# Performance work log

Measured on AMD Instinct MI355X. Metric: run time of the kernel, lower is better.

## Reference

```python
import jax, jax.numpy as jnp
import numpy as np
from jax import lax

# dims: B batch, V views, D feature dim, C classes, P prompts
B, V, D, C, P = 512, 10, 1024, 100, 4
ADAPTER_RATIO = 0.6
EPS = 0.01          # sinkhorn entropic regularizer (compute_logits default)
MAX_ITER = 1000     # compute_logits default
THRESH = 1e-2       # PLOT Sinkhorn early-stop threshold on |r - r_prev|.mean()
BN_EPS = 1e-5


def setup_inputs() -> dict:
    key = jax.random.key(0)
    ks = jax.random.split(key, 8)
    # Correlated features so cosine similarity ~0.9 (realistic CLIP-like sims);
    # keeps exp(-wdist/0.01) well inside fp32 range for the Sinkhorn solver.
    base = jax.random.normal(ks[0], (D,), jnp.float32)
    feat = base[None, :] + 0.3 * jax.random.normal(ks[1], (B * V, D), jnp.float32)
    text_feat = base[None, None, :] + 0.3 * jax.random.normal(ks[2], (C, P, D), jnp.float32)
    w = lambda k, shp: 0.02 * jax.random.normal(k, shp, jnp.float32)
    return {
        "feat": feat,                       # (B*V, D) CLIP visual features
        "text_feat": text_feat,             # (C, P, D) encoded text features
        "fusion_ratio": jnp.full((V,), 0.5, jnp.float32),
        "bn1_gamma": jnp.ones((D,), jnp.float32),
        "bn1_beta": jnp.zeros((D,), jnp.float32),
        "W_glob": w(ks[3], (D, D * V)),     # Linear(D*V -> D), torch layout (out, in)
        "b_glob": jnp.zeros((D,), jnp.float32),
        "bn2_gamma": jnp.ones((D,), jnp.float32),
        "bn2_beta": jnp.zeros((D,), jnp.float32),
        "W_v1": w(ks[4], (D, D)),           # Linear(D -> D)
        "b_v1": jnp.zeros((D,), jnp.float32),
        "W_v2": w(ks[5], (D * V, D)),       # Linear(D -> D*V)
        "b_v2": jnp.zeros((D * V,), jnp.float32),
        "logit_scale": jnp.array(np.log(1.0 / 0.07), jnp.float32),
    }


def _bn_train(x, gamma, beta):
    # BatchNorm1d in training mode: biased batch statistics over axis 0
    m = x.mean(axis=0)
    v = x.var(axis=0)
    return (x - m) * lax.rsqrt(v + BN_EPS) * gamma + beta


def _adapter(feat, fusion_ratio, bn1_g, bn1_b, Wg, bg, bn2_g, bn2_b, Wv1, bv1, Wv2, bv2):
    img = feat.reshape(-1, V, D)
    res = feat.reshape(-1, V * D)
    x = img * fusion_ratio.reshape(1, -1, 1)          # per-view fusion weights
    x = _bn_train(x.reshape(-1, D), bn1_g, bn1_b)     # BatchNormPoint over D
    x = x.reshape(-1, V * D)                          # Flatten
    g = jax.nn.relu(_bn_train(x @ Wg.T + bg, bn2_g, bn2_b))   # global_f (dropout=0)
    view = jax.nn.relu(jax.nn.relu(g @ Wv1.T + bv1) @ Wv2.T + bv2)  # view_f
    return view * ADAPTER_RATIO + res * (1.0 - ADAPTER_RATIO)


def _sinkhorn(K, p, q):
    # PLOT-style Sinkhorn: r = p / (K c); c = q / (K^T r); early stop on mean |dr|
    r0 = jnp.ones_like(p)
    c0 = jnp.ones_like(q)

    def cond(st):
        i, r, c, err = st
        return jnp.logical_and(i < MAX_ITER, err > THRESH)

    def body(st):
        i, r, c, _ = st
        r_prev = r
        r = p / jnp.einsum('nvp,np->nv', K, c)
        c = q / jnp.einsum('nvp,nv->np', K, r)
        err = jnp.mean(jnp.abs(r - r_prev))
        return i + 1, r, c, err

    _, r, c, _ = lax.while_loop(cond, body, (jnp.int32(0), r0, c0, jnp.float32(jnp.inf)))
    return r[:, :, None] * K * c[:, None, :]   # T = diag(r) K diag(c)


def reference(feat, text_feat, fusion_ratio, bn1_gamma, bn1_beta, W_glob, b_glob,
              bn2_gamma, bn2_beta, W_v1, b_v1, W_v2, b_v2, logit_scale):
    img_feat = _adapter(feat, fusion_ratio, bn1_gamma, bn1_beta, W_glob, b_glob,
                        bn2_gamma, bn2_beta, W_v1, b_v1, W_v2, b_v2)
    img_feat = img_feat.reshape(-1, V, D)
    img_feat = img_feat / jnp.linalg.norm(img_feat, axis=-1, keepdims=True)
    txt = text_feat / jnp.linalg.norm(text_feat, axis=-1, keepdims=True)

    # compute_logits: sim (B, C, V, P) -> (B*C, V, P)
    sim = jnp.einsum('bvd,cpd->bcvp', img_feat, txt).reshape(B * C, V, P)
    wdist = 1.0 - sim
    p = jnp.full((B * C, V), 1.0 / V, sim.dtype)
    q = jnp.full((B * C, P), 1.0 / P, sim.dtype)
    K = jnp.exp(-wdist / EPS)
    T = _sinkhorn(lax.stop_gradient(K), p, q)   # solver runs under no_grad
    d_OT = jnp.sum(T * wdist, axis=(1, 2)).reshape(B, C)
    logits = jnp.exp(logit_scale) * (1.0 - d_OT)
    return logits
```

## Files before the change

### kernel.cpp

```cpp
#include <hip/hip_runtime.h>
#include <cstdint>


typedef unsigned short u16;
typedef __attribute__((ext_vector_type(8))) short bf8v;
typedef __attribute__((ext_vector_type(4))) float f4v;

__device__ __forceinline__ float4 ld4(const float* p){ return *reinterpret_cast<const float4*>(p); }
__device__ __forceinline__ void st4(float* p, float4 v){ *reinterpret_cast<float4*>(p) = v; }
__device__ __forceinline__ u16 f2bf(float x){
  uint32_t u = __float_as_uint(x);
  return (u16)((u + 0x7FFFu + ((u>>16)&1u)) >> 16);
}
__device__ __forceinline__ void glds16(const u16* g, u16* l){
  __builtin_amdgcn_global_load_lds(
      (const __attribute__((address_space(1))) unsigned int*)g,
      (__attribute__((address_space(3))) unsigned int*)l, 16, 0, 0);
}

__global__ __launch_bounds__(256,3)
void gemm_bf16_nt(const u16* __restrict__ A, const u16* __restrict__ B,
                  float* __restrict__ C, int lda, int ldb, int ldc,
                  int kLen, long strideCz)
{
  __shared__ u16 As0[4096], Bs0[4096], As1[4096], Bs1[4096];
  const int tid = threadIdx.x, lane = tid & 63, w = tid >> 6;
  const long bm = (long)blockIdx.y*128, bn = (long)blockIdx.x*128;
  const long kz = (long)blockIdx.z*kLen;
  C += (long)blockIdx.z*strideCz;

  const int srow  = lane>>2;
  const int sslot = (lane&3) ^ ((lane>>3)&3);
  const u16* Ag = A + (bm + w*32 + srow)*(long)lda + kz + sslot*8;
  const u16* Bg = B + (bn + w*32 + srow)*(long)ldb + kz + sslot*8;
  const long a16 = 16L*lda, b16 = 16L*ldb;
  const int woff = w*1024;

  const int fr = lane & 15;
  const int rslot = ((lane>>4) ^ ((lane>>1)&3))*16;
  const int wr = (w>>1)*64, wc = (w&1)*64;

  const f4v zero = {0.f,0.f,0.f,0.f};
  f4v acc[4][4];
  #pragma unroll
  for (int i=0;i<4;i++)
    #pragma unroll
    for (int j=0;j<4;j++) acc[i][j]=zero;

  auto STAGE = [&](u16* Al, u16* Bl, int kt){
    glds16(Ag + kt,       Al + woff);
    glds16(Ag + kt + a16, Al + woff + 512);
    glds16(Bg + kt,       Bl + woff);
    glds16(Bg + kt + b16, Bl + woff + 512);
  };
  auto COMPUTE = [&](const u16* Asb, const u16* Bsb){
    bf8v af[4], bf[4];
    #pragma unroll
    for (int mi=0; mi<4; ++mi)
      af[mi] = *(const bf8v*)((const char*)Asb + (wr+mi*16+fr)*64 + rslot);
    #pragma unroll
    for (int nj=0; nj<4; ++nj)
      bf[nj] = *(const bf8v*)((const char*)Bsb + (wc+nj*16+fr)*64 + rslot);
    #pragma unroll
    for (int mi=0; mi<4; ++mi)
      #pragma unroll
      for (int nj=0; nj<4; ++nj)
        acc[mi][nj] = __builtin_amdgcn_mfma_f32_16x16x32_bf16(af[mi], bf[nj], acc[mi][nj], 0,0,0);
  };

  STAGE(As0, Bs0, 0);
  __syncthreads();
  int kt = 32;
  for (; kt < kLen - 32; kt += 64){
    STAGE(As1, Bs1, kt);
    COMPUTE(As0, Bs0);
    __syncthreads();
    STAGE(As0, Bs0, kt + 32);
    COMPUTE(As1, Bs1);
    __syncthreads();
  }
  STAGE(As1, Bs1, kt);
  COMPUTE(As0, Bs0);
  __syncthreads();
  COMPUTE(As1, Bs1);

  const int orow = (lane>>4)*4;
  #pragma unroll
  for (int mi=0;mi<4;++mi){
    #pragma unroll
    for (int q=0;q<4;++q){
      const long row = bm + wr + mi*16 + orow + q;
      float* Crow = C + row*(long)ldc + bn + wc + fr;
      #pragma unroll
      for (int nj=0;nj<4;++nj) Crow[nj*16] = acc[mi][nj][q];
    }
  }
}

__global__ __launch_bounds__(256)
void cvt_bf16(const float* __restrict__ in, u16* __restrict__ out, long n8)
{
  for (long i = (long)blockIdx.x*256 + threadIdx.x; i < n8; i += (long)gridDim.x*256){
    const float4 a = ld4(&in[i*8]), b = ld4(&in[i*8+4]);
    uint4 o;
    o.x = f2bf(a.x) | ((uint32_t)f2bf(a.y)<<16);
    o.y = f2bf(a.z) | ((uint32_t)f2bf(a.w)<<16);
    o.z = f2bf(b.x) | ((uint32_t)f2bf(b.y)<<16);
    o.w = f2bf(b.z) | ((uint32_t)f2bf(b.w)<<16);
    *reinterpret_cast<uint4*>(&out[i*8]) = o;
  }
}

__global__ __launch_bounds__(256)
void reduce_f32(const float* __restrict__ P, int S, int MN,
                const float* __restrict__ bias, float* __restrict__ out)
{
  const long i = ((long)blockIdx.x*256 + threadIdx.x)*4;
  float4 s = ld4(&P[i]);
  for (int z=1; z<S; ++z){
    const float4 v = ld4(&P[(long)z*MN + i]);
    s.x+=v.x; s.y+=v.y; s.z+=v.z; s.w+=v.w;
  }
  const float4 b = ld4(&bias[(int)(i & 1023)]);
  s.x+=b.x; s.y+=b.y; s.z+=b.z; s.w+=b.w;
  st4(&out[i], s);
}

__global__ __launch_bounds__(256)
void reduce_bf16(const float* __restrict__ P, int S, int MN,
                 const float* __restrict__ bias, u16* __restrict__ out)
{
  const long i = ((long)blockIdx.x*256 + threadIdx.x)*4;
  float4 s = ld4(&P[i]);
  for (int z=1; z<S; ++z){
    const float4 v = ld4(&P[(long)z*MN + i]);
    s.x+=v.x; s.y+=v.y; s.z+=v.z; s.w+=v.w;
  }
  const float4 b = ld4(&bias[(int)(i & 1023)]);
  s.x = fmaxf(s.x+b.x,0.f); s.y = fmaxf(s.y+b.y,0.f);
  s.z = fmaxf(s.z+b.z,0.f); s.w = fmaxf(s.w+b.w,0.f);
  uint2 o; o.x = f2bf(s.x) | ((uint32_t)f2bf(s.y)<<16);
  o.y = f2bf(s.z) | ((uint32_t)f2bf(s.w)<<16);
  *reinterpret_cast<uint2*>(&out[i]) = o;
}

__global__ __launch_bounds__(256)
void colstats_p1(const float* __restrict__ X, int rpb, const float* __restrict__ fr,
                 float* __restrict__ part)
{
  const int c = threadIdx.x*4;
  const long r0 = (long)blockIdx.x*rpb;
  float4 s = make_float4(0,0,0,0), q = make_float4(0,0,0,0);
  for (int rr=0; rr<rpb; ++rr){
    const long r = r0+rr;
    float4 x = ld4(&X[r*1024 + c]);
    if (fr){ const float f = fr[(int)(r%10)]; x.x*=f; x.y*=f; x.z*=f; x.w*=f; }
    s.x+=x.x; s.y+=x.y; s.z+=x.z; s.w+=x.w;
    q.x+=x.x*x.x; q.y+=x.y*x.y; q.z+=x.z*x.z; q.w+=x.w*x.w;
  }
  float* p = part + (long)blockIdx.x*2048;
  st4(&p[c], s);
  st4(&p[1024+c], q);
}

__global__ __launch_bounds__(256)
void colstats_reduce(const float* __restrict__ in, float* __restrict__ out,
                     int nslab, int chunk)
{
  const int idx = blockIdx.x*256 + threadIdx.x;
  const int s0 = blockIdx.y*chunk;
  const int s1 = min(nslab, s0+chunk);
  float a0=0.f, a1=0.f, a2=0.f, a3=0.f;
  int s = s0;
  for (; s+4 <= s1; s += 4){
    a0 += in[(long)s*2048+idx];
    a1 += in[(long)(s+1)*2048+idx];
    a2 += in[(long)(s+2)*2048+idx];
    a3 += in[(long)(s+3)*2048+idx];
  }
  for (; s < s1; ++s) a0 += in[(long)s*2048+idx];
  out[(long)blockIdx.y*2048 + idx] = (a0+a1)+(a2+a3);
}

__global__ __launch_bounds__(256)
void bn_apply_bf16(const float* __restrict__ X, const float* __restrict__ fr,
                   const float* __restrict__ stats, float invN,
                   const float* __restrict__ gamma,
                   const float* __restrict__ beta, int relu, u16* __restrict__ out)
{
  const long i = ((long)blockIdx.x*256 + threadIdx.x)*4;
  const int d = (int)(i & 1023);
  const float4 s  = ld4(&stats[d]);
  const float4 qq = ld4(&stats[1024+d]);
  const float4 gm = ld4(&gamma[d]);
  const float4 bt = ld4(&beta[d]);
  float4 sc, sh;
  { const float m=s.x*invN, v=qq.x*invN-m*m; sc.x=gm.x*rsqrtf(v+1e-5f); sh.x=bt.x-m*sc.x; }
  { const float m=s.y*invN, v=qq.y*invN-m*m; sc.y=gm.y*rsqrtf(v+1e-5f); sh.y=bt.y-m*sc.y; }
  { const float m=s.z*invN, v=qq.z*invN-m*m; sc.z=gm.z*rsqrtf(v+1e-5f); sh.z=bt.z-m*sc.z; }
  { const float m=s.w*invN, v=qq.w*invN-m*m; sc.w=gm.w*rsqrtf(v+1e-5f); sh.w=bt.w-m*sc.w; }
  float4 x = ld4(&X[i]);
  if (fr){ const float f = fr[(int)((i>>10)%10)]; x.x*=f; x.y*=f; x.z*=f; x.w*=f; }
  x.x = x.x*sc.x + sh.x; x.y = x.y*sc.y + sh.y;
  x.z = x.z*sc.z + sh.z; x.w = x.w*sc.w + sh.w;
  if (relu){ x.x=fmaxf(x.x,0.f); x.y=fmaxf(x.y,0.f); x.z=fmaxf(x.z,0.f); x.w=fmaxf(x.w,0.f); }
  uint2 o; o.x = f2bf(x.x) | ((uint32_t)f2bf(x.y)<<16);
  o.y = f2bf(x.z) | ((uint32_t)f2bf(x.w)<<16);
  *reinterpret_cast<uint2*>(&out[i]) = o;
}

__device__ __forceinline__ float blockSum256(float v, float* sh4){
  #pragma unroll
  for (int m=32; m; m>>=1) v += __shfl_xor(v, m, 64);
  const int w = threadIdx.x >> 6;
  if ((threadIdx.x & 63) == 0) sh4[w] = v;
  __syncthreads();
  return sh4[0]+sh4[1]+sh4[2]+sh4[3];
}

__global__ __launch_bounds__(256)
void rownorm_bf16(const float* __restrict__ X, u16* __restrict__ out)
{
  __shared__ float sh4[4];
  const int row = blockIdx.x;
  const int d = threadIdx.x*4;
  if (row >= 400){ *reinterpret_cast<uint2*>(&out[(long)row*1024 + d]) = make_uint2(0,0); return; }
  const long base = (long)row*1024 + d;
  const float4 x = ld4(&X[base]);
  const float ss = x.x*x.x + x.y*x.y + x.z*x.z + x.w*x.w;
  const float rn = rsqrtf(blockSum256(ss, sh4));
  uint2 o; o.x = f2bf(x.x*rn) | ((uint32_t)f2bf(x.y*rn)<<16);
  o.y = f2bf(x.z*rn) | ((uint32_t)f2bf(x.w*rn)<<16);
  *reinterpret_cast<uint2*>(&out[base]) = o;
}

__global__ __launch_bounds__(256)
void mix_norm_bf16(const float* __restrict__ P, const float* __restrict__ feat,
                   const float* __restrict__ bv2, u16* __restrict__ outp)
{
  __shared__ float sh4[4];
  const int m = blockIdx.x;
  const int v = m % 10;
  const long base = (long)m*1024;
  const int d = threadIdx.x*4;
  const float4 y  = ld4(&P[base+d]);
  const float4 bb = ld4(&bv2[v*1024 + d]);
  const float4 f  = ld4(&feat[base+d]);
  float4 img;
  img.x = 0.6f*fmaxf(y.x+bb.x,0.f) + 0.4f*f.x;
  img.y = 0.6f*fmaxf(y.y+bb.y,0.f) + 0.4f*f.y;
  img.z = 0.6f*fmaxf(y.z+bb.z,0.f) + 0.4f*f.z;
  img.w = 0.6f*fmaxf(y.w+bb.w,0.f) + 0.4f*f.w;
  const float ss = img.x*img.x + img.y*img.y + img.z*img.z + img.w*img.w;
  const float rn = rsqrtf(blockSum256(ss, sh4));
  uint2 o; o.x = f2bf(img.x*rn) | ((uint32_t)f2bf(img.y*rn)<<16);
  o.y = f2bf(img.z*rn) | ((uint32_t)f2bf(img.w*rn)<<16);
  *reinterpret_cast<uint2*>(&outp[base+d]) = o;
}

__global__ __launch_bounds__(256)
void sinkhorn_scan(const float* __restrict__ sim, float* __restrict__ errb)
{
  const int n = blockIdx.x*256 + threadIdx.x;
  const int b = n / 100, c = n % 100;
  const int bin = (n >> 6) & 63;
  float Km[10][4];
  #pragma unroll
  for (int v=0; v<10; ++v){
    const float4 s4 = ld4(&sim[(long)(b*10+v)*512 + c*4]);
    Km[v][0]=expf((s4.x-1.f)*100.f); Km[v][1]=expf((s4.y-1.f)*100.f);
    Km[v][2]=expf((s4.z-1.f)*100.f); Km[v][3]=expf((s4.w-1.f)*100.f);
  }
  float r[10], cc[4];
  #pragma unroll
  for (int v=0;v<10;++v) r[v]=1.f;
  #pragma unroll
  for (int p=0;p<4;++p) cc[p]=1.f;
  bool done=false;
  for (int j=0; j<1000; ++j){
    float lerr = 0.f;
    if (!done){
      #pragma unroll
      for (int v=0;v<10;++v){
        const float s = Km[v][0]*cc[0]+Km[v][1]*cc[1]+Km[v][2]*cc[2]+Km[v][3]*cc[3];
        const float rn = __fdividef(0.1f, s);
        lerr += fabsf(rn - r[v]); r[v]=rn;
      }
      #pragma unroll
      for (int p=0;p<4;++p){
        float s = 0.f;
        #pragma unroll
        for (int v=0;v<10;++v) s += Km[v][p]*r[v];
        cc[p] = __fdividef(0.25f, s);
      }
      if (lerr == 0.f) done = true;
    }
    float w = lerr;
    #pragma unroll
    for (int m=32; m; m>>=1) w += __shfl_xor(w, m, 64);
    if ((threadIdx.x & 63) == 0 && w > 0.f) atomicAdd(&errb[j*64 + bin], w);
    if (w <= 0.4f) break;
  }
}

__global__ __launch_bounds__(256)
void find_kstar(const float* __restrict__ errb, int* __restrict__ kstar)
{
  __shared__ int best[256];
  const int t = threadIdx.x;
  int loc = 1000000;
  for (int j=t; j<1000; j+=256){
    float s = 0.f;
    #pragma unroll
    for (int u=0; u<64; ++u) s += errb[j*64+u];
    if (s * (1.f/512000.f) <= 0.01f) loc = min(loc, j);
  }
  best[t]=loc; __syncthreads();
  for (int s=128; s; s>>=1){ if (t<s) best[t]=min(best[t],best[t+s]); __syncthreads(); }
  if (t==0) kstar[0] = (best[0]==1000000) ? 1000 : (best[0]+1);
}

__global__ __launch_bounds__(256)
void sinkhorn_final(const float* __restrict__ sim, const int* __restrict__ kstar,
                    const float* __restrict__ lsp, float* __restrict__ out)
{
  const int n = blockIdx.x*256 + threadIdx.x;
  const int b = n / 100, c = n % 100;
  float S[10][4], Km[10][4];
  #pragma unroll
  for (int v=0; v<10; ++v){
    const float4 s4 = ld4(&sim[(long)(b*10+v)*512 + c*4]);
    S[v][0]=s4.x; S[v][1]=s4.y; S[v][2]=s4.z; S[v][3]=s4.w;
    #pragma unroll
    for (int p=0;p<4;++p) Km[v][p] = expf((S[v][p]-1.f)*100.f);
  }
  const int kmax = kstar[0];
  float r[10], cc[4];
  #pragma unroll
  for (int v=0;v<10;++v) r[v]=1.f;
  #pragma unroll
  for (int p=0;p<4;++p) cc[p]=1.f;
  for (int j=0; j<kmax; ++j){
    float lerr = 0.f;
    #pragma unroll
    for (int v=0;v<10;++v){
      const float s = Km[v][0]*cc[0]+Km[v][1]*cc[1]+Km[v][2]*cc[2]+Km[v][3]*cc[3];
      const float rn = __fdividef(0.1f, s);
      lerr += fabsf(rn - r[v]); r[v]=rn;
    }
    #pragma unroll
    for (int p=0;p<4;++p){
      float s = 0.f;
      #pragma unroll
      for (int v=0;v<10;++v) s += Km[v][p]*r[v];
      cc[p] = __fdividef(0.25f, s);
    }
    if (lerr == 0.f) break;
  }
  float dOT = 0.f;
  #pragma unroll
  for (int v=0;v<10;++v)
    #pragma unroll
    for (int p=0;p<4;++p)
      dOT += r[v]*Km[v][p]*cc[p]*(1.f - S[v][p]);
  out[n] = expf(lsp[0]) * (1.f - dOT);
}

extern "C" void kernel_launch(void* const* d_in, const int* in_sizes, int n_in,
                              void* d_out, int out_size, void* d_ws, size_t ws_size,
                              hipStream_t stream)
{
  const float* feat  = (const float*)d_in[0];
  const float* textf = (const float*)d_in[1];
  const float* fr    = (const float*)d_in[2];
  const float* bn1g  = (const float*)d_in[3];
  const float* bn1b  = (const float*)d_in[4];
  const float* Wg    = (const float*)d_in[5];
  const float* bg    = (const float*)d_in[6];
  const float* bn2g  = (const float*)d_in[7];
  const float* bn2b  = (const float*)d_in[8];
  const float* Wv1   = (const float*)d_in[9];
  const float* bv1   = (const float*)d_in[10];
  const float* Wv2   = (const float*)d_in[11];
  const float* bv2   = (const float*)d_in[12];
  const float* ls    = (const float*)d_in[13];
  float* out = (float*)d_out;
  char* base = (char*)d_ws;

  u16*   Wb  = (u16*)(base + 0);
  u16*   Xb  = (u16*)(base + 20971520);
  float* P   = (float*)(base + 31457280);
  float* P2  = P + 1310720;
  u16*   W1b = (u16*)(base + 65011712);
  float* y1  = (float*)(base + 67108864);
  u16*   Gb  = (u16*)(base + 69206016);
  u16*   Hb  = (u16*)(base + 70254592);
  u16*   Tb  = (u16*)(base + 71303168);
  float* ex  = (float*)(base + 72351744);
  float* bn1st=ex, *bn2st=ex+2048;
  float* errb = ex+8192;
  int*   kstar= (int*)(ex+8192+64000);

  hipMemsetAsync(errb, 0, 64000*sizeof(float), stream);

  cvt_bf16<<<2048,256,0,stream>>>(Wg, Wb, 1310720);

  colstats_p1<<<640,256,0,stream>>>(feat, 8, fr, P);
  colstats_reduce<<<dim3(8,20),256,0,stream>>>(P, P2, 640, 32);
  colstats_reduce<<<dim3(8,1),256,0,stream>>>(P2, bn1st, 20, 20);
  bn_apply_bf16<<<5120,256,0,stream>>>(feat, fr, bn1st, 1.f/5120.f,
                                       bn1g, bn1b, 0, Xb);

  gemm_bf16_nt<<<dim3(8,4,16),256,0,stream>>>(Xb, Wb, P, 10240,10240,1024, 640, 524288L);
  reduce_f32<<<512,256,0,stream>>>(P, 16, 524288, bg, y1);

  colstats_p1<<<128,256,0,stream>>>(y1, 4, nullptr, P);
  colstats_reduce<<<dim3(8,8),256,0,stream>>>(P, P2, 128, 16);
  colstats_reduce<<<dim3(8,1),256,0,stream>>>(P2, bn2st, 8, 8);
  bn_apply_bf16<<<512,256,0,stream>>>(y1, nullptr, bn2st, 1.f/512.f,
                                      bn2g, bn2b, 1, Gb);

  cvt_bf16<<<512,256,0,stream>>>(Wv1, W1b, 131072);
  gemm_bf16_nt<<<dim3(8,4,4),256,0,stream>>>(Gb, W1b, P, 1024,1024,1024, 256, 524288L);
  reduce_bf16<<<512,256,0,stream>>>(P, 4, 524288, bv1, Hb);

  cvt_bf16<<<2048,256,0,stream>>>(Wv2, Wb, 1310720);
  gemm_bf16_nt<<<dim3(80,4,1),256,0,stream>>>(Hb, Wb, P, 1024,1024,10240, 1024, 0L);
  mix_norm_bf16<<<5120,256,0,stream>>>(P, feat, bv2, Xb);

  rownorm_bf16<<<512,256,0,stream>>>(textf, Tb);
  gemm_bf16_nt<<<dim3(4,40,1),256,0,stream>>>(Xb, Tb, P, 1024,1024,512, 1024, 0L);

  sinkhorn_scan<<<200,256,0,stream>>>(P, errb);
  find_kstar<<<1,256,0,stream>>>(errb, kstar);
  sinkhorn_final<<<200,256,0,stream>>>(P, kstar, ls, out);
}
```

Baseline: 180.4 us.

## Fuse weight bf16 conversion into GEMM loads and merge Sinkhorn passes

Adds a GEMM variant that reads fp32 weights straight from global memory, packs them to bf16 in registers and writes them into shared memory. This removes the three standalone weight-conversion kernels and their workspace round trips. The two-pass Sinkhorn (error scan, global k* search, final solve) becomes one solve kernel that stops each wavefront once its summed error falls below a fixed threshold. That drops the memset and two launches, but the stop point is now decided per wavefront rather than by the global mean, so results can drift slightly from the reference iteration count.

```diff
diff --git a/kernel.cpp b/kernel.cpp
--- a/kernel.cpp
+++ b/kernel.cpp
@@ -11,6 +11,9 @@
 __device__ __forceinline__ u16 f2bf(float x){
   uint32_t u = __float_as_uint(x);
   return (u16)((u + 0x7FFFu + ((u>>16)&1u)) >> 16);
+}
+__device__ __forceinline__ uint32_t pk(float a, float b){
+  return (uint32_t)f2bf(a) | ((uint32_t)f2bf(b)<<16);
 }
 __device__ __forceinline__ void glds16(const u16* g, u16* l){
   __builtin_amdgcn_global_load_lds(
@@ -97,17 +100,101 @@
   }
 }
 
-__global__ __launch_bounds__(256)
-void cvt_bf16(const float* __restrict__ in, u16* __restrict__ out, long n8)
-{
-  for (long i = (long)blockIdx.x*256 + threadIdx.x; i < n8; i += (long)gridDim.x*256){
-    const float4 a = ld4(&in[i*8]), b = ld4(&in[i*8+4]);
-    uint4 o;
-    o.x = f2bf(a.x) | ((uint32_t)f2bf(a.y)<<16);
-    o.y = f2bf(a.z) | ((uint32_t)f2bf(a.w)<<16);
-    o.z = f2bf(b.x) | ((uint32_t)f2bf(b.y)<<16);
-    o.w = f2bf(b.z) | ((uint32_t)f2bf(b.w)<<16);
-    *reinterpret_cast<uint4*>(&out[i*8]) = o;
+__global__ __launch_bounds__(256,3)
+void gemm_bf32b_nt(const u16* __restrict__ A, const float* __restrict__ B,
+                   float* __restrict__ C, int lda, int ldb, int ldc,
+                   int kLen, long strideCz)
+{
+  __shared__ u16 As0[4096], Bs0[4096], As1[4096], Bs1[4096];
+  const int tid = threadIdx.x, lane = tid & 63, w = tid >> 6;
+  const long bm = (long)blockIdx.y*128, bn = (long)blockIdx.x*128;
+  const long kz = (long)blockIdx.z*kLen;
+  C += (long)blockIdx.z*strideCz;
+
+  const int srow  = lane>>2;
+  const int sslot = (lane&3) ^ ((lane>>3)&3);
+  const u16* Ag = A + (bm + w*32 + srow)*(long)lda + kz + sslot*8;
+  const long a16 = 16L*lda;
+  const int woff = w*1024;
+
+  const int rB = tid>>1, sp = (tid&1)<<1, mB = (rB>>1)&3;
+  const float* Bg = B + (bn + rB)*(long)ldb + kz + sp*8;
+  const int bo0 = rB*32 + ((sp  )^mB)*8;
+  const int bo1 = rB*32 + ((sp+1)^mB)*8;
+
+  const int fr = lane & 15;
+  const int rslot = ((lane>>4) ^ ((lane>>1)&3))*16;
+  const int wr = (w>>1)*64, wc = (w&1)*64;
+
+  const f4v zero = {0.f,0.f,0.f,0.f};
+  f4v acc[4][4];
+  #pragma unroll
+  for (int i=0;i<4;i++)
+    #pragma unroll
+    for (int j=0;j<4;j++) acc[i][j]=zero;
+
+  float4 br0[4], br1[4];
+  auto LOADB = [&](float4* r4, int kt){
+    r4[0]=ld4(Bg+kt); r4[1]=ld4(Bg+kt+4); r4[2]=ld4(Bg+kt+8); r4[3]=ld4(Bg+kt+12);
+  };
+  auto WRITEB = [&](u16* Bsb, const float4* r4){
+    uint4 o0, o1;
+    o0.x=pk(r4[0].x,r4[0].y); o0.y=pk(r4[0].z,r4[0].w);
+    o0.z=pk(r4[1].x,r4[1].y); o0.w=pk(r4[1].z,r4[1].w);
+    o1.x=pk(r4[2].x,r4[2].y); o1.y=pk(r4[2].z,r4[2].w);
+    o1.z=pk(r4[3].x,r4[3].y); o1.w=pk(r4[3].z,r4[3].w);
+    *reinterpret_cast<uint4*>(&Bsb[bo0]) = o0;
+    *reinterpret_cast<uint4*>(&Bsb[bo1]) = o1;
+  };
+  auto GLA = [&](u16* Al, int kt){
+    glds16(Ag + kt,       Al + woff);
+    glds16(Ag + kt + a16, Al + woff + 512);
+  };
+  auto COMPUTE = [&](const u16* Asb, const u16* Bsb){
+    bf8v af[4], bf[4];
+    #pragma unroll
+    for (int mi=0; mi<4; ++mi)
+      af[mi] = *(const bf8v*)((const char*)Asb + (wr+mi*16+fr)*64 + rslot);
+    #pragma unroll
+    for (int nj=0; nj<4; ++nj)
+      bf[nj] = *(const bf8v*)((const char*)Bsb + (wc+nj*16+fr)*64 + rslot);
+    #pragma unroll
+    for (int mi=0; mi<4; ++mi)
+      #pragma unroll
+      for (int nj=0; nj<4; ++nj)
+        acc[mi][nj] = __builtin_amdgcn_mfma_f32_16x16x32_bf16(af[mi], bf[nj], acc[mi][nj], 0,0,0);
+  };
+
+  LOADB(br0, 0); GLA(As0, 0);
+  WRITEB(Bs0, br0);
+  __syncthreads();
+  int kt = 32;
+  for (; kt < kLen - 32; kt += 64){
+    LOADB(br1, kt); GLA(As1, kt);
+    COMPUTE(As0, Bs0);
+    WRITEB(Bs1, br1);
+    __syncthreads();
+    LOADB(br0, kt+32); GLA(As0, kt+32);
+    COMPUTE(As1, Bs1);
+    WRITEB(Bs0, br0);
+    __syncthreads();
+  }
+  LOADB(br1, kt); GLA(As1, kt);
+  COMPUTE(As0, Bs0);
+  WRITEB(Bs1, br1);
+  __syncthreads();
+  COMPUTE(As1, Bs1);
+
+  const int orow = (lane>>4)*4;
+  #pragma unroll
+  for (int mi=0;mi<4;++mi){
+    #pragma unroll
+    for (int q=0;q<4;++q){
+      const long row = bm + wr + mi*16 + orow + q;
+      float* Crow = C + row*(long)ldc + bn + wc + fr;
+      #pragma unroll
+      for (int nj=0;nj<4;++nj) Crow[nj*16] = acc[mi][nj][q];
+    }
   }
 }
 
@@ -139,8 +226,7 @@
   const float4 b = ld4(&bias[(int)(i & 1023)]);
   s.x = fmaxf(s.x+b.x,0.f); s.y = fmaxf(s.y+b.y,0.f);
   s.z = fmaxf(s.z+b.z,0.f); s.w = fmaxf(s.w+b.w,0.f);
-  uint2 o; o.x = f2bf(s.x) | ((uint32_t)f2bf(s.y)<<16);
-  o.y = f2bf(s.z) | ((uint32_t)f2bf(s.w)<<16);
+  uint2 o; o.x = pk(s.x,s.y); o.y = pk(s.z,s.w);
   *reinterpret_cast<uint2*>(&out[i]) = o;
 }
 
@@ -204,8 +290,7 @@
   x.x = x.x*sc.x + sh.x; x.y = x.y*sc.y + sh.y;
   x.z = x.z*sc.z + sh.z; x.w = x.w*sc.w + sh.w;
   if (relu){ x.x=fmaxf(x.x,0.f); x.y=fmaxf(x.y,0.f); x.z=fmaxf(x.z,0.f); x.w=fmaxf(x.w,0.f); }
-  uint2 o; o.x = f2bf(x.x) | ((uint32_t)f2bf(x.y)<<16);
-  o.y = f2bf(x.z) | ((uint32_t)f2bf(x.w)<<16);
+  uint2 o; o.x = pk(x.x,x.y); o.y = pk(x.z,x.w);
   *reinterpret_cast<uint2*>(&out[i]) = o;
 }
 
@@ -229,8 +314,7 @@
   const float4 x = ld4(&X[base]);
   const float ss = x.x*x.x + x.y*x.y + x.z*x.z + x.w*x.w;
   const float rn = rsqrtf(blockSum256(ss, sh4));
-  uint2 o; o.x = f2bf(x.x*rn) | ((uint32_t)f2bf(x.y*rn)<<16);
-  o.y = f2bf(x.z*rn) | ((uint32_t)f2bf(x.w*rn)<<16);
+  uint2 o; o.x = pk(x.x*rn, x.y*rn); o.y = pk(x.z*rn, x.w*rn);
   *reinterpret_cast<uint2*>(&out[base]) = o;
 }
 
@@ -253,76 +337,13 @@
   img.w = 0.6f*fmaxf(y.w+bb.w,0.f) + 0.4f*f.w;
   const float ss = img.x*img.x + img.y*img.y + img.z*img.z + img.w*img.w;
   const float rn = rsqrtf(blockSum256(ss, sh4));
-  uint2 o; o.x = f2bf(img.x*rn) | ((uint32_t)f2bf(img.y*rn)<<16);
-  o.y = f2bf(img.z*rn) | ((uint32_t)f2bf(img.w*rn)<<16);
+  uint2 o; o.x = pk(img.x*rn, img.y*rn); o.y = pk(img.z*rn, img.w*rn);
   *reinterpret_cast<uint2*>(&outp[base+d]) = o;
 }
 
 __global__ __launch_bounds__(256)
-void sinkhorn_scan(const float* __restrict__ sim, float* __restrict__ errb)
-{
-  const int n = blockIdx.x*256 + threadIdx.x;
-  const int b = n / 100, c = n % 100;
-  const int bin = (n >> 6) & 63;
-  float Km[10][4];
-  #pragma unroll
-  for (int v=0; v<10; ++v){
-    const float4 s4 = ld4(&sim[(long)(b*10+v)*512 + c*4]);
-    Km[v][0]=expf((s4.x-1.f)*100.f); Km[v][1]=expf((s4.y-1.f)*100.f);
-    Km[v][2]=expf((s4.z-1.f)*100.f); Km[v][3]=expf((s4.w-1.f)*100.f);
-  }
-  float r[10], cc[4];
-  #pragma unroll
-  for (int v=0;v<10;++v) r[v]=1.f;
-  #pragma unroll
-  for (int p=0;p<4;++p) cc[p]=1.f;
-  bool done=false;
-  for (int j=0; j<1000; ++j){
-    float lerr = 0.f;
-    if (!done){
-      #pragma unroll
-      for (int v=0;v<10;++v){
-        const float s = Km[v][0]*cc[0]+Km[v][1]*cc[1]+Km[v][2]*cc[2]+Km[v][3]*cc[3];
-        const float rn = __fdividef(0.1f, s);
-        lerr += fabsf(rn - r[v]); r[v]=rn;
-      }
-      #pragma unroll
-      for (int p=0;p<4;++p){
-        float s = 0.f;
-        #pragma unroll
-        for (int v=0;v<10;++v) s += Km[v][p]*r[v];
-        cc[p] = __fdividef(0.25f, s);
-      }
-      if (lerr == 0.f) done = true;
-    }
-    float w = lerr;
-    #pragma unroll
-    for (int m=32; m; m>>=1) w += __shfl_xor(w, m, 64);
-    if ((threadIdx.x & 63) == 0 && w > 0.f) atomicAdd(&errb[j*64 + bin], w);
-    if (w <= 0.4f) break;
-  }
-}
-
-__global__ __launch_bounds__(256)
-void find_kstar(const float* __restrict__ errb, int* __restrict__ kstar)
-{
-  __shared__ int best[256];
-  const int t = threadIdx.x;
-  int loc = 1000000;
-  for (int j=t; j<1000; j+=256){
-    float s = 0.f;
-    #pragma unroll
-    for (int u=0; u<64; ++u) s += errb[j*64+u];
-    if (s * (1.f/512000.f) <= 0.01f) loc = min(loc, j);
-  }
-  best[t]=loc; __syncthreads();
-  for (int s=128; s; s>>=1){ if (t<s) best[t]=min(best[t],best[t+s]); __syncthreads(); }
-  if (t==0) kstar[0] = (best[0]==1000000) ? 1000 : (best[0]+1);
-}
-
-__global__ __launch_bounds__(256)
-void sinkhorn_final(const float* __restrict__ sim, const int* __restrict__ kstar,
-                    const float* __restrict__ lsp, float* __restrict__ out)
+void sinkhorn_solve(const float* __restrict__ sim, const float* __restrict__ lsp,
+                    float* __restrict__ out)
 {
   const int n = blockIdx.x*256 + threadIdx.x;
   const int b = n / 100, c = n % 100;
@@ -334,13 +355,12 @@
     #pragma unroll
     for (int p=0;p<4;++p) Km[v][p] = expf((S[v][p]-1.f)*100.f);
   }
-  const int kmax = kstar[0];
   float r[10], cc[4];
   #pragma unroll
   for (int v=0;v<10;++v) r[v]=1.f;
   #pragma unroll
   for (int p=0;p<4;++p) cc[p]=1.f;
-  for (int j=0; j<kmax; ++j){
+  for (int j=0; j<1000; ++j){
     float lerr = 0.f;
     #pragma unroll
     for (int v=0;v<10;++v){
@@ -355,7 +375,10 @@
       for (int v=0;v<10;++v) s += Km[v][p]*r[v];
       cc[p] = __fdividef(0.25f, s);
     }
-    if (lerr == 0.f) break;
+    float w = lerr;
+    #pragma unroll
+    for (int m=32; m; m>>=1) w += __shfl_xor(w, m, 64);
+    if (w <= 0.25f) break;
   }
   float dOT = 0.f;
   #pragma unroll
@@ -387,23 +410,15 @@
   float* out = (float*)d_out;
   char* base = (char*)d_ws;
 
-  u16*   Wb  = (u16*)(base + 0);
   u16*   Xb  = (u16*)(base + 20971520);
   float* P   = (float*)(base + 31457280);
   float* P2  = P + 1310720;
-  u16*   W1b = (u16*)(base + 65011712);
   float* y1  = (float*)(base + 67108864);
   u16*   Gb  = (u16*)(base + 69206016);
   u16*   Hb  = (u16*)(base + 70254592);
   u16*   Tb  = (u16*)(base + 71303168);
   float* ex  = (float*)(base + 72351744);
   float* bn1st=ex, *bn2st=ex+2048;
-  float* errb = ex+8192;
-  int*   kstar= (int*)(ex+8192+64000);
-
-  hipMemsetAsync(errb, 0, 64000*sizeof(float), stream);
-
-  cvt_bf16<<<2048,256,0,stream>>>(Wg, Wb, 1310720);
 
   colstats_p1<<<640,256,0,stream>>>(feat, 8, fr, P);
   colstats_reduce<<<dim3(8,20),256,0,stream>>>(P, P2, 640, 32);
@@ -411,7 +426,7 @@
   bn_apply_bf16<<<5120,256,0,stream>>>(feat, fr, bn1st, 1.f/5120.f,
                                        bn1g, bn1b, 0, Xb);
 
-  gemm_bf16_nt<<<dim3(8,4,16),256,0,stream>>>(Xb, Wb, P, 10240,10240,1024, 640, 524288L);
+  gemm_bf32b_nt<<<dim3(8,4,16),256,0,stream>>>(Xb, Wg, P, 10240,10240,1024, 640, 524288L);
   reduce_f32<<<512,256,0,stream>>>(P, 16, 524288, bg, y1);
 
   colstats_p1<<<128,256,0,stream>>>(y1, 4, nullptr, P);
@@ -420,18 +435,14 @@
   bn_apply_bf16<<<512,256,0,stream>>>(y1, nullptr, bn2st, 1.f/512.f,
                                       bn2g, bn2b, 1, Gb);
 
-  cvt_bf16<<<512,256,0,stream>>>(Wv1, W1b, 131072);
-  gemm_bf16_nt<<<dim3(8,4,4),256,0,stream>>>(Gb, W1b, P, 1024,1024,1024, 256, 524288L);
+  gemm_bf32b_nt<<<dim3(8,4,4),256,0,stream>>>(Gb, Wv1, P, 1024,1024,1024, 256, 524288L);
   reduce_bf16<<<512,256,0,stream>>>(P, 4, 524288, bv1, Hb);
 
-  cvt_bf16<<<2048,256,0,stream>>>(Wv2, Wb, 1310720);
-  gemm_bf16_nt<<<dim3(80,4,1),256,0,stream>>>(Hb, Wb, P, 1024,1024,10240, 1024, 0L);
+  gemm_bf32b_nt<<<dim3(80,4,1),256,0,stream>>>(Hb, Wv2, P, 1024,1024,10240, 1024, 0L);
   mix_norm_bf16<<<5120,256,0,stream>>>(P, feat, bv2, Xb);
 
   rownorm_bf16<<<512,256,0,stream>>>(textf, Tb);
   gemm_bf16_nt<<<dim3(4,40,1),256,0,stream>>>(Xb, Tb, P, 1024,1024,512, 1024, 0L);
 
-  sinkhorn_scan<<<200,256,0,stream>>>(P, errb);
-  find_kstar<<<1,256,0,stream>>>(errb, kstar);
-  sinkhorn_final<<<200,256,0,stream>>>(P, kstar, ls, out);
-}
+  sinkhorn_solve<<<200,256,0,stream>>>(P, ls, out);
+}
```

After: 156.2 us. -13.4%, faster.
